# Performance work log

Measured on AMD Instinct MI355X. Metric: run time of the kernel, lower is better.

## Reference

```python
import jax, jax.numpy as jnp
import numpy as np
from jax import lax

SEQ_LEN = 15
LATENT = 16
HIDDEN = 64
OUT = 1
BATCH = 65536


def setup_inputs() -> dict:
    key = jax.random.key(0)
    ks = jax.random.split(key, 11)
    s = lambda *shape: 1.0 / np.sqrt(HIDDEN)
    def u(k, shape):
        return jax.random.uniform(k, shape, jnp.float32, -1.0 / np.sqrt(HIDDEN), 1.0 / np.sqrt(HIDDEN))
    return {
        "z": jax.random.normal(ks[0], (BATCH, LATENT), jnp.float32),
        "Wih0": u(ks[1], (4 * HIDDEN, LATENT)),
        "Whh0": u(ks[2], (4 * HIDDEN, HIDDEN)),
        "bih0": u(ks[3], (4 * HIDDEN,)),
        "bhh0": u(ks[4], (4 * HIDDEN,)),
        "Wih1": u(ks[5], (4 * HIDDEN, HIDDEN)),
        "Whh1": u(ks[6], (4 * HIDDEN, HIDDEN)),
        "bih1": u(ks[7], (4 * HIDDEN,)),
        "bhh1": u(ks[8], (4 * HIDDEN,)),
        "Wfc": u(ks[9], (OUT, HIDDEN)),
        "bfc": u(ks[10], (OUT,)),
    }


def lstm_layer(x, Wih, Whh, bih, bhh):
    # x: [B, T, D]. PyTorch gate order: i, f, g, o.
    B, T, _ = x.shape
    H = Whh.shape[1]
    # precompute input projections for all timesteps: [T, B, 4H]
    x_proj = jnp.einsum('btd,gd->tbg', x, Wih) + (bih + bhh)

    def step(carry, xp):
        h, c = carry
        gates = xp + h @ Whh.T
        i, f, g, o = jnp.split(gates, 4, axis=-1)
        i = jax.nn.sigmoid(i)
        f = jax.nn.sigmoid(f)
        g = jnp.tanh(g)
        o = jax.nn.sigmoid(o)
        c = f * c + i * g
        h = o * jnp.tanh(c)
        return (h, c), h

    h0 = jnp.zeros((B, H), x.dtype)
    _, ys = lax.scan(step, (h0, h0), x_proj)  # ys: [T, B, H]
    return jnp.swapaxes(ys, 0, 1)  # [B, T, H]


def reference(z, Wih0, Whh0, bih0, bhh0, Wih1, Whh1, bih1, bhh1, Wfc, bfc):
    # z: [B, latent] -> repeat along time: [B, T, latent]
    x = jnp.broadcast_to(z[:, None, :], (z.shape[0], SEQ_LEN, z.shape[1]))
    h1 = lstm_layer(x, Wih0, Whh0, bih0, bhh0)
    # (inter-layer dropout is inactive in eval mode)
    h2 = lstm_layer(h1, Wih1, Whh1, bih1, bhh1)
    return h2 @ Wfc.T + bfc  # [B, T, OUT]
```

## Files before the change

kernel.cpp:

```cpp
#include <hip/hip_runtime.h>

#define TSTEPS 15
#define HID    64
#define LAT    16
#define NBATCH 65536
#define LOG2E  1.44269504088896f

typedef _Float16 v8h __attribute__((ext_vector_type(8)));
typedef _Float16 v4h __attribute__((ext_vector_type(4)));
typedef _Float16 v2h __attribute__((ext_vector_type(2)));
typedef float    v4f __attribute__((ext_vector_type(4)));

__device__ __forceinline__ v8h vzero8() {
    v8h v;
#pragma unroll
    for (int i = 0; i < 8; ++i) v[i] = (_Float16)0.0f;
    return v;
}

__device__ __forceinline__ v4h pack4(float a, float b, float c, float d) {
    const v2h lo = __builtin_bit_cast(v2h, __builtin_amdgcn_cvt_pkrtz(a, b));
    const v2h hi = __builtin_bit_cast(v2h, __builtin_amdgcn_cvt_pkrtz(c, d));
    return __builtin_shufflevector(lo, hi, 0, 1, 2, 3);
}

__device__ __forceinline__ float cell_update(float ai, float af, float ag,
                                             float ao, float& cst) {
    const float ei = __builtin_amdgcn_exp2f(-ai);
    const float ef = __builtin_amdgcn_exp2f(-af);
    const float eg = __builtin_amdgcn_exp2f(-ag);
    const float eo = __builtin_amdgcn_exp2f(-ao);
    const float p1  = (1.0f + ei) * (1.0f + eg);
    const float pf  = 1.0f + ef;
    const float num = fmaf(cst, p1, (1.0f - eg) * pf);
    const float cc  = num * __builtin_amdgcn_rcpf(p1 * pf);
    cst = cc;
    const float ec = __builtin_amdgcn_exp2f(cc * (-2.0f * LOG2E));
    return (1.0f - ec) *
        __builtin_amdgcn_rcpf((1.0f + eo) * (1.0f + ec));
}

__global__ __launch_bounds__(1024)
__attribute__((amdgpu_waves_per_eu(4, 4)))
void lstm2_pipe7(
        const float* __restrict__ z,
        const float* __restrict__ Wih0, const float* __restrict__ Whh0,
        const float* __restrict__ bih0, const float* __restrict__ bhh0,
        const float* __restrict__ Wih1, const float* __restrict__ Whh1,
        const float* __restrict__ bih1, const float* __restrict__ bhh1,
        const float* __restrict__ Wfc,  const float* __restrict__ bfc,
        float* __restrict__ out)
{
    __shared__ __align__(16) _Float16 wf[7 * 16 * 64 * 8];
    __shared__ __align__(16) _Float16 wfcf[2 * 64 * 8];
    __shared__ __align__(16) float    bsum1[256];
    __shared__ __align__(16) _Float16 state[16][16 * 72];

    const int tid  = threadIdx.x;
    const int wave = tid >> 6;
    const int lane = tid & 63;
    const int q    = lane >> 4;
    const int c    = lane & 15;
    const int row0 = blockIdx.x * 256 + wave * 16;

#pragma unroll 2
    for (int e = tid; e < 7 * 16 * 64 * 8; e += 1024) {
        const int j  = e & 7;
        const int lm = (e >> 3) & 63;
        const int mt = (e >> 9) & 15;
        const int p  = e >> 13;
        const int g  = mt * 16 + (lm & 15);
        const int kk = (lm >> 4) * 8 + j;
        float v;
        if (p == 0)      v = (kk < LAT) ? Wih0[g * LAT + kk]
                           : (kk == LAT ? bih0[g] + bhh0[g] : 0.0f);
        else if (p == 1) v = Whh0[g * HID + kk];
        else if (p == 2) v = Whh0[g * HID + 32 + kk];
        else if (p == 3) v = Wih1[g * HID + kk];
        else if (p == 4) v = Wih1[g * HID + 32 + kk];
        else if (p == 5) v = Whh1[g * HID + kk];
        else             v = Whh1[g * HID + 32 + kk];
        const float sc = ((g >> 6) == 2) ? (2.0f * LOG2E) : LOG2E;
        wf[e] = (_Float16)(v * sc);
    }
    if (tid < 2 * 64 * 8) {
        const int e  = tid;
        const int j  = e & 7;
        const int lm = (e >> 3) & 63;
        const int kc = e >> 9;
        const int kk = kc * 32 + (lm >> 4) * 8 + j;
        wfcf[e] = ((lm & 15) == 0) ? (_Float16)Wfc[kk] : (_Float16)0.0f;
    }
    if (tid < 256)
        bsum1[tid] = (bih1[tid] + bhh1[tid]) *
                     (((tid >> 6) == 2) ? (2.0f * LOG2E) : LOG2E);
    __syncthreads();

    _Float16* stW = &state[wave][0];
    const float bfcv = bfc[0];

    const v8h wfc0 = *(const v8h*)&wfcf[(0 * 64 + lane) * 8];
    const v8h wfc1 = *(const v8h*)&wfcf[(1 * 64 + lane) * 8];

    v8h zfrag = vzero8();
    if (q < 2) {
        const float* zp = z + (size_t)(row0 + c) * LAT + q * 8;
        const float4 za = *(const float4*)(zp);
        const float4 zb = *(const float4*)(zp + 4);
        zfrag[0] = (_Float16)za.x; zfrag[1] = (_Float16)za.y;
        zfrag[2] = (_Float16)za.z; zfrag[3] = (_Float16)za.w;
        zfrag[4] = (_Float16)zb.x; zfrag[5] = (_Float16)zb.y;
        zfrag[6] = (_Float16)zb.z; zfrag[7] = (_Float16)zb.w;
    }
    if (q == 2) zfrag[0] = (_Float16)1.0f;

    v8h hf0 = vzero8(), hf1 = vzero8();
    v8h gf0 = vzero8(), gf1 = vzero8();
    v4h h1pk[4];
    float c0s[16], c1s[16];
#pragma unroll
    for (int i = 0; i < 16; ++i) { c0s[i] = 0.0f; c1s[i] = 0.0f; }

#define AFRAG(pl, mt) (*(const v8h*)&wf[(((pl) * 16 + (mt)) * 64 + lane) * 8])
#define MFMA16(A, B, C) __builtin_amdgcn_mfma_f32_16x16x32_f16((A), (B), (C), 0, 0, 0)

    auto l0_part = [&]() {
#pragma unroll
        for (int a = 0; a < 4; ++a) {
            v4f acc0[4];
            __builtin_amdgcn_s_setprio(1);
#pragma unroll
            for (int ty = 0; ty < 4; ++ty) {
                const int mt = 4 * ty + a;
                v4f t0 = {0.f, 0.f, 0.f, 0.f};
                t0 = MFMA16(AFRAG(0, mt), zfrag, t0);
                t0 = MFMA16(AFRAG(1, mt), hf0,   t0);
                t0 = MFMA16(AFRAG(2, mt), hf1,   t0);
                acc0[ty] = t0;
            }
            __builtin_amdgcn_s_setprio(0);
            float hh[4];
#pragma unroll
            for (int r = 0; r < 4; ++r)
                hh[r] = cell_update(acc0[0][r], acc0[1][r], acc0[2][r],
                                    acc0[3][r], c0s[a * 4 + r]);
            *(v4h*)&stW[c * 72 + 16 * a + 4 * q] = pack4(hh[0], hh[1], hh[2], hh[3]);
        }
    };

    auto l1_part = [&]() {
#pragma unroll
        for (int a = 0; a < 4; ++a) {
            v4f acc1[4];
            __builtin_amdgcn_s_setprio(1);
#pragma unroll
            for (int ty = 0; ty < 4; ++ty) {
                const int mt = 4 * ty + a;
                v4f t0 = *(const v4f*)&bsum1[64 * ty + 16 * a + 4 * q];
                t0 = MFMA16(AFRAG(3, mt), hf0, t0);
                t0 = MFMA16(AFRAG(4, mt), hf1, t0);
                t0 = MFMA16(AFRAG(5, mt), gf0, t0);
                t0 = MFMA16(AFRAG(6, mt), gf1, t0);
                acc1[ty] = t0;
            }
            __builtin_amdgcn_s_setprio(0);
            float hh[4];
#pragma unroll
            for (int r = 0; r < 4; ++r)
                hh[r] = cell_update(acc1[0][r], acc1[1][r], acc1[2][r],
                                    acc1[3][r], c1s[a * 4 + r]);
            h1pk[a] = pack4(hh[0], hh[1], hh[2], hh[3]);
        }
    };

    auto l0_finish = [&]() {
        hf0 = *(const v8h*)&stW[c * 72 + 8 * q];
        hf1 = *(const v8h*)&stW[c * 72 + 32 + 8 * q];
    };

    auto l1_finish = [&](int trow) {
#pragma unroll
        for (int a = 0; a < 4; ++a)
            *(v4h*)&stW[c * 72 + 16 * a + 4 * q] = h1pk[a];
        gf0 = *(const v8h*)&stW[c * 72 + 8 * q];
        gf1 = *(const v8h*)&stW[c * 72 + 32 + 8 * q];
        v4f f = {0.f, 0.f, 0.f, 0.f};
        f = MFMA16(wfc0, gf0, f);
        f = MFMA16(wfc1, gf1, f);
        if (lane < 16)
            out[(size_t)(row0 + lane) * TSTEPS + trow] = f[0] + bfcv;
    };

    l0_part();
    l0_finish();

#pragma unroll 1
    for (int tt = 1; tt < TSTEPS; ++tt) {
        __asm__ __volatile__("" ::: "memory");
        l0_part();
        l1_part();
        l0_finish();
        l1_finish(tt - 1);
    }

    __asm__ __volatile__("" ::: "memory");
    l1_part();
    l1_finish(TSTEPS - 1);

#undef AFRAG
#undef MFMA16
}

extern "C" void kernel_launch(void* const* d_in, const int* in_sizes, int n_in,
                              void* d_out, int out_size, void* d_ws, size_t ws_size,
                              hipStream_t stream)
{
    (void)in_sizes; (void)n_in; (void)out_size; (void)d_ws; (void)ws_size;

    const float* z    = (const float*)d_in[0];
    const float* Wih0 = (const float*)d_in[1];
    const float* Whh0 = (const float*)d_in[2];
    const float* bih0 = (const float*)d_in[3];
    const float* bhh0 = (const float*)d_in[4];
    const float* Wih1 = (const float*)d_in[5];
    const float* Whh1 = (const float*)d_in[6];
    const float* bih1 = (const float*)d_in[7];
    const float* bhh1 = (const float*)d_in[8];
    const float* Wfc  = (const float*)d_in[9];
    const float* bfc  = (const float*)d_in[10];

    lstm2_pipe7<<<dim3(NBATCH / 256), dim3(1024), 0, stream>>>(
        z, Wih0, Whh0, bih0, bhh0, Wih1, Whh1, bih1, bhh1, Wfc, bfc,
        (float*)d_out);
}
```

Baseline: 250.0 us.

## Defer FC output by a step, pad state stride, drop setprio

Splits the layer-1 finish into a state store and a separate FC output step. The FC MFMA and global store for step t-2 now run after the next layer-0 part, which takes them off the critical path right after the LDS round trip. Also changes the LDS state row stride from 72 to 74 halves to alter the bank mapping, and removes the s_setprio hints around the MFMA blocks. Risks: the stride-74 row offset is only 4-byte aligned, so the 8- and 16-byte vector LDS accesses may split into narrower ones, and dropping priority hints may hurt interleaving between waves.

```diff
diff --git a/kernel.cpp b/kernel.cpp
--- a/kernel.cpp
+++ b/kernel.cpp
@@ -5,6 +5,7 @@
 #define LAT    16
 #define NBATCH 65536
 #define LOG2E  1.44269504088896f
+#define SSTR   74
 
 typedef _Float16 v8h __attribute__((ext_vector_type(8)));
 typedef _Float16 v4h __attribute__((ext_vector_type(4)));
@@ -42,7 +43,7 @@
 
 __global__ __launch_bounds__(1024)
 __attribute__((amdgpu_waves_per_eu(4, 4)))
-void lstm2_pipe7(
+void lstm2_pipe8(
         const float* __restrict__ z,
         const float* __restrict__ Wih0, const float* __restrict__ Whh0,
         const float* __restrict__ bih0, const float* __restrict__ bhh0,
@@ -54,7 +55,7 @@
     __shared__ __align__(16) _Float16 wf[7 * 16 * 64 * 8];
     __shared__ __align__(16) _Float16 wfcf[2 * 64 * 8];
     __shared__ __align__(16) float    bsum1[256];
-    __shared__ __align__(16) _Float16 state[16][16 * 72];
+    __shared__ __align__(16) _Float16 state[16][16 * SSTR];
 
     const int tid  = threadIdx.x;
     const int wave = tid >> 6;
@@ -128,7 +129,6 @@
 #pragma unroll
         for (int a = 0; a < 4; ++a) {
             v4f acc0[4];
-            __builtin_amdgcn_s_setprio(1);
 #pragma unroll
             for (int ty = 0; ty < 4; ++ty) {
                 const int mt = 4 * ty + a;
@@ -138,13 +138,13 @@
                 t0 = MFMA16(AFRAG(2, mt), hf1,   t0);
                 acc0[ty] = t0;
             }
-            __builtin_amdgcn_s_setprio(0);
             float hh[4];
 #pragma unroll
             for (int r = 0; r < 4; ++r)
                 hh[r] = cell_update(acc0[0][r], acc0[1][r], acc0[2][r],
                                     acc0[3][r], c0s[a * 4 + r]);
-            *(v4h*)&stW[c * 72 + 16 * a + 4 * q] = pack4(hh[0], hh[1], hh[2], hh[3]);
+            *(v4h*)&stW[c * SSTR + 16 * a + 4 * q] =
+                pack4(hh[0], hh[1], hh[2], hh[3]);
         }
     };
 
@@ -152,7 +152,6 @@
 #pragma unroll
         for (int a = 0; a < 4; ++a) {
             v4f acc1[4];
-            __builtin_amdgcn_s_setprio(1);
 #pragma unroll
             for (int ty = 0; ty < 4; ++ty) {
                 const int mt = 4 * ty + a;
@@ -163,7 +162,6 @@
                 t0 = MFMA16(AFRAG(6, mt), gf1, t0);
                 acc1[ty] = t0;
             }
-            __builtin_amdgcn_s_setprio(0);
             float hh[4];
 #pragma unroll
             for (int r = 0; r < 4; ++r)
@@ -174,16 +172,19 @@
     };
 
     auto l0_finish = [&]() {
-        hf0 = *(const v8h*)&stW[c * 72 + 8 * q];
-        hf1 = *(const v8h*)&stW[c * 72 + 32 + 8 * q];
-    };
-
-    auto l1_finish = [&](int trow) {
+        hf0 = *(const v8h*)&stW[c * SSTR + 8 * q];
+        hf1 = *(const v8h*)&stW[c * SSTR + 32 + 8 * q];
+    };
+
+    auto l1_store_gf = [&]() {
 #pragma unroll
         for (int a = 0; a < 4; ++a)
-            *(v4h*)&stW[c * 72 + 16 * a + 4 * q] = h1pk[a];
-        gf0 = *(const v8h*)&stW[c * 72 + 8 * q];
-        gf1 = *(const v8h*)&stW[c * 72 + 32 + 8 * q];
+            *(v4h*)&stW[c * SSTR + 16 * a + 4 * q] = h1pk[a];
+        gf0 = *(const v8h*)&stW[c * SSTR + 8 * q];
+        gf1 = *(const v8h*)&stW[c * SSTR + 32 + 8 * q];
+    };
+
+    auto fc_out = [&](int trow) {
         v4f f = {0.f, 0.f, 0.f, 0.f};
         f = MFMA16(wfc0, gf0, f);
         f = MFMA16(wfc1, gf1, f);
@@ -194,18 +195,27 @@
     l0_part();
     l0_finish();
 
+    __asm__ __volatile__("" ::: "memory");
+    l0_part();
+    l1_part();
+    l0_finish();
+    l1_store_gf();
+
 #pragma unroll 1
-    for (int tt = 1; tt < TSTEPS; ++tt) {
+    for (int tt = 2; tt < TSTEPS; ++tt) {
         __asm__ __volatile__("" ::: "memory");
         l0_part();
+        fc_out(tt - 2);
         l1_part();
         l0_finish();
-        l1_finish(tt - 1);
+        l1_store_gf();
     }
 
     __asm__ __volatile__("" ::: "memory");
     l1_part();
-    l1_finish(TSTEPS - 1);
+    fc_out(TSTEPS - 2);
+    l1_store_gf();
+    fc_out(TSTEPS - 1);
 
 #undef AFRAG
 #undef MFMA16
@@ -229,7 +239,7 @@
     const float* Wfc  = (const float*)d_in[9];
     const float* bfc  = (const float*)d_in[10];
 
-    lstm2_pipe7<<<dim3(NBATCH / 256), dim3(1024), 0, stream>>>(
+    lstm2_pipe8<<<dim3(NBATCH / 256), dim3(1024), 0, stream>>>(
         z, Wih0, Whh0, bih0, bhh0, Wih1, Whh1, bih1, bhh1, Wfc, bfc,
         (float*)d_out);
 }
```

After: 284.7 us. 1.14x slower.
